# Kernel optimization log

Measured on AMD Instinct MI355X. Metric: run time of the kernel, lower is better.

## Reference

```python
import jax, jax.numpy as jnp
import numpy as np

B, NV, NH = 256, 512, 256


def setup_inputs() -> dict:
    key = jax.random.key(0)
    k1, k2, k3, k4, k5 = jax.random.split(key, 5)
    return {
        "wt": jax.random.normal(k1, (B, NH, NV), dtype=jnp.float32),
        "varh_diag": jax.random.uniform(k2, (B, NH), dtype=jnp.float32),
        "sig2": jax.random.uniform(k3, (B,), dtype=jnp.float32),
        "b": jax.random.normal(k4, (B, NV), dtype=jnp.float32),
        "muh": jax.random.normal(k5, (B, NH), dtype=jnp.float32),
    }


def reference(wt, varh_diag, sig2, b, muh):
    # wt: [B, nh, nv], varh_diag: [B, nh], sig2: [B], b: [B, nv], muh: [B, nh]
    nv = wt.shape[2]
    w = jnp.transpose(wt, (0, 2, 1))                      # [B, nv, nh]
    # diag(varh_diag) @ wt == broadcasted row scaling (avoids materializing diag)
    varvh = varh_diag[:, :, None] * wt                    # [B, nh, nv]
    # varv = w @ varh @ wt + sig2 * I
    varv = jnp.einsum('bvh,bhu->bvu', w, varvh)           # [B, nv, nv]
    varv = varv + sig2[:, None, None] * jnp.eye(nv, dtype=wt.dtype)
    # muv = b + w @ muh
    muv = b + jnp.einsum('bvh,bh->bv', w, muh)            # [B, nv]
    mu = jnp.concatenate([muv, muh], axis=1)              # [B, nv+nh]
    # block covariance: [[varv, varvh^T], [varvh, diag(varh_diag)]]
    varh = jax.vmap(jnp.diag)(varh_diag)                  # [B, nh, nh]
    varvht = jnp.transpose(varvh, (0, 2, 1))              # [B, nv, nh]
    top = jnp.concatenate([varv, varvht], axis=2)         # [B, nv, nv+nh]
    bot = jnp.concatenate([varvh, varh], axis=2)          # [B, nh, nv+nh]
    var = jnp.concatenate([top, bot], axis=1)             # [B, nv+nh, nv+nh]
    return mu, var
```

## Files before the change

kernel.cpp:

```cpp
#include <hip/hip_runtime.h>
#include <hip/hip_bf16.h>

#define B_  256
#define NH  256
#define NV  512
#define NT  768
#define TILES_PER_BATCH 22

typedef __bf16 bf16x8 __attribute__((ext_vector_type(8)));
typedef float  f32x4  __attribute__((ext_vector_type(4)));

__device__ __forceinline__ __bf16 f2bf(float f) { return static_cast<__bf16>(f); }

__global__ __launch_bounds__(256) void fused(const float* __restrict__ wt,
                                             const float* __restrict__ varh,
                                             const float* __restrict__ sig2,
                                             const float* __restrict__ bvec,
                                             const float* __restrict__ muh,
                                             float* __restrict__ out) {
    __shared__ __align__(16) char smem[38 * 1024];

    const int bid  = blockIdx.x;
    const int q    = bid >> 3;
    const int b    = (bid & 7) * 32 + q / TILES_PER_BATCH;
    const int tile = q % TILES_PER_BATCH;
    const int t    = threadIdx.x;

    const float* wtb  = wt + (size_t)b * NH * NV;
    float* mu   = out + (size_t)b * NT;
    float* varb = out + (size_t)B_ * NT + (size_t)b * NT * NT;

    if (tile < 10) {
        static const signed char MT[10] = {0,1,2,3, 0,0,0,1,1,2};
        static const signed char NTc[10] = {0,1,2,3, 1,2,3,2,3,3};
        const int mt = MT[tile], nt = NTc[tile];
        const bool diag = (mt == nt);

        bf16x8 (*As)[128]  = (bf16x8(*)[128])(smem);
        bf16x8 (*Bs)[128]  = (bf16x8(*)[128])(smem + 16 * 1024);
        float*  varh_s     = (float*)(smem + 32 * 1024);
        float*  muh_s      = (float*)(smem + 33 * 1024);
        float (*red)[128]  = (float(*)[128])(smem + 34 * 1024);

        const int m0 = mt * 128, n0 = nt * 128;
        const int lane = t & 63, wid = t >> 6;
        const int wm = wid >> 1, wn = wid & 1;
        const int mc = t & 31;
        const int kb = t >> 5;

        varh_s[t] = varh[b * NH + t];
        muh_s[t]  = muh[b * NH + t];

        f32x4 acc[4][4] = {};
        float acc_mu[4] = {0.f, 0.f, 0.f, 0.f};
        __syncthreads();

        for (int st = 0; st < 4; ++st) {
            const int k0 = st * 64;
            f32x4 av[8], bv[8];
            const float* baseA = wtb + (size_t)(k0 + kb * 8) * NV + m0 + 4 * mc;
#pragma unroll
            for (int j = 0; j < 8; ++j)
                av[j] = *reinterpret_cast<const f32x4*>(baseA + j * NV);
            if (!diag) {
                const float* baseB = wtb + (size_t)(k0 + kb * 8) * NV + n0 + 4 * mc;
#pragma unroll
                for (int j = 0; j < 8; ++j)
                    bv[j] = *reinterpret_cast<const f32x4*>(baseB + j * NV);
            } else {
#pragma unroll
                for (int j = 0; j < 8; ++j) bv[j] = av[j];
            }
            float sc[8];
#pragma unroll
            for (int j = 0; j < 8; ++j) sc[j] = varh_s[k0 + kb * 8 + j];

            if (diag) {
#pragma unroll
                for (int j = 0; j < 8; ++j) {
                    const float mh = muh_s[k0 + kb * 8 + j];
#pragma unroll
                    for (int mj = 0; mj < 4; ++mj) acc_mu[mj] += av[j][mj] * mh;
                }
            }

            if (st) __syncthreads();

#pragma unroll
            for (int mj = 0; mj < 4; ++mj) {
                bf16x8 pa, pb;
#pragma unroll
                for (int j = 0; j < 8; ++j) {
                    pa[j] = f2bf(av[j][mj]);
                    pb[j] = f2bf(bv[j][mj] * sc[j]);
                }
                const int ca = 4 * mc + mj;
                const int ci = ca ^ ((ca >> 3) & 7);
                As[kb][ci] = pa;
                Bs[kb][ci] = pb;
            }
            __syncthreads();

#pragma unroll
            for (int kh = 0; kh < 2; ++kh) {
                const int ko = kh * 4 + (lane >> 4);
                bf16x8 af[4], bfr[4];
#pragma unroll
                for (int f = 0; f < 4; ++f) {
                    const int mi = wm * 64 + f * 16 + (lane & 15);
                    af[f] = As[ko][mi ^ ((mi >> 3) & 7)];
                    const int ni = wn * 64 + f * 16 + (lane & 15);
                    bfr[f] = Bs[ko][ni ^ ((ni >> 3) & 7)];
                }
#pragma unroll
                for (int fm = 0; fm < 4; ++fm)
#pragma unroll
                    for (int fn = 0; fn < 4; ++fn)
                        acc[fm][fn] = __builtin_amdgcn_mfma_f32_16x16x32_bf16(
                            af[fm], bfr[fn], acc[fm][fn], 0, 0, 0);
            }
        }

        const float s2 = sig2[b];
#pragma unroll
        for (int fm = 0; fm < 4; ++fm) {
#pragma unroll
            for (int fn = 0; fn < 4; ++fn) {
                const int row = m0 + wm * 64 + fm * 16 + ((lane >> 4) << 2);
                const int col = n0 + wn * 64 + fn * 16 + (lane & 15);
#pragma unroll
                for (int r = 0; r < 4; ++r) {
                    float v = acc[fm][fn][r];
                    if (row + r == col) v += s2;
                    varb[(size_t)(row + r) * NT + col] = v;
                }
                if (!diag) {
                    *reinterpret_cast<f32x4*>(varb + (size_t)col * NT + row) =
                        acc[fm][fn];
                }
            }
        }

        if (diag) {
#pragma unroll
            for (int mj = 0; mj < 4; ++mj) red[kb][4 * mc + mj] = acc_mu[mj];
            __syncthreads();
            if (t < 128) {
                float s = 0.f;
#pragma unroll
                for (int k = 0; k < 8; ++k) s += red[k][t];
                mu[m0 + t] = bvec[b * NV + m0 + t] + s;
            }
        }
    } else if (tile < 18) {
        const int idx = tile - 10;
        const int hi = idx >> 2, vj = idx & 3;
        const int h0 = hi * 128, v0 = vj * 128;
        float (*tl)[65] = (float(*)[65])smem;
        const int r  = t >> 4;
        const int c4 = (t & 15) * 4;

        for (int sub = 0; sub < 4; ++sub) {
            const int sh = (sub >> 1) * 64, sv = (sub & 1) * 64;
            if (sub) __syncthreads();
#pragma unroll
            for (int p = 0; p < 4; ++p) {
                const int h = h0 + sh + r + 16 * p;
                const float vh = varh[b * NH + h];
                f32x4 x = *reinterpret_cast<const f32x4*>(
                    wtb + (size_t)h * NV + v0 + sv + c4);
                x *= vh;
                *reinterpret_cast<f32x4*>(
                    varb + (size_t)(NV + h) * NT + v0 + sv + c4) = x;
                tl[r + 16 * p][c4 + 0] = x[0];
                tl[r + 16 * p][c4 + 1] = x[1];
                tl[r + 16 * p][c4 + 2] = x[2];
                tl[r + 16 * p][c4 + 3] = x[3];
            }
            __syncthreads();
#pragma unroll
            for (int p = 0; p < 4; ++p) {
                const int vrow = v0 + sv + r + 16 * p;
                f32x4 y;
                y[0] = tl[c4 + 0][r + 16 * p];
                y[1] = tl[c4 + 1][r + 16 * p];
                y[2] = tl[c4 + 2][r + 16 * p];
                y[3] = tl[c4 + 3][r + 16 * p];
                *reinterpret_cast<f32x4*>(
                    varb + (size_t)vrow * NT + NV + h0 + sh + c4) = y;
            }
        }
    } else {
        const int d  = tile - 18;
        const int di = d >> 1, dj = d & 1;
        const int r0 = NV + di * 128, c0 = NV + dj * 128;
        const int rr = t >> 5;
        const int c4 = (t & 31) * 4;
#pragma unroll
        for (int p = 0; p < 16; ++p) {
            const int row = rr + 8 * p;
            f32x4 v = {0.f, 0.f, 0.f, 0.f};
            if (di == dj) {
                const int dpos = row - c4;
                if (dpos >= 0 && dpos < 4) v[dpos] = varh[b * NH + di * 128 + row];
            }
            *reinterpret_cast<f32x4*>(varb + (size_t)(r0 + row) * NT + c0 + c4) = v;
        }
        if (d == 0) mu[NV + t] = muh[b * NH + t];
    }
}

extern "C" void kernel_launch(void* const* d_in, const int* in_sizes, int n_in,
                              void* d_out, int out_size, void* d_ws, size_t ws_size,
                              hipStream_t stream) {
    (void)in_sizes; (void)n_in; (void)out_size; (void)d_ws; (void)ws_size;
    const float* wt   = (const float*)d_in[0];
    const float* varh = (const float*)d_in[1];
    const float* sig2 = (const float*)d_in[2];
    const float* bvec = (const float*)d_in[3];
    const float* muh  = (const float*)d_in[4];
    float* out = (float*)d_out;

    fused<<<B_ * TILES_PER_BATCH, 256, 0, stream>>>(wt, varh, sig2, bvec, muh, out);
}
```

Measured before the change: 162.4 us.

## Enlarge tiles to 256x256 with 512-thread blocks, 9 tiles per batch

The varv GEMM now uses three 256x256 upper-triangle tiles per batch instead of ten 128x128 tiles, run by 512-thread blocks with 8x4 MFMA accumulators per wave. The copy and diagonal tiles are resized to match, and the block count per batch drops from 22 to 9. This cuts redundant global reads of wt across tiles and the per-block overhead. In exchange, register pressure and LDS use (76KB) per block rise, which lowers occupancy, and the coarser tiles give fewer blocks to balance across CUs.

```diff
diff --git a/kernel.cpp b/kernel.cpp
--- a/kernel.cpp
+++ b/kernel.cpp
@@ -5,53 +5,51 @@
 #define NH  256
 #define NV  512
 #define NT  768
-#define TILES_PER_BATCH 22
+#define TPB 9
 
 typedef __bf16 bf16x8 __attribute__((ext_vector_type(8)));
 typedef float  f32x4  __attribute__((ext_vector_type(4)));
 
 __device__ __forceinline__ __bf16 f2bf(float f) { return static_cast<__bf16>(f); }
 
-__global__ __launch_bounds__(256) void fused(const float* __restrict__ wt,
+__global__ __launch_bounds__(512) void fused(const float* __restrict__ wt,
                                              const float* __restrict__ varh,
                                              const float* __restrict__ sig2,
                                              const float* __restrict__ bvec,
                                              const float* __restrict__ muh,
                                              float* __restrict__ out) {
-    __shared__ __align__(16) char smem[38 * 1024];
+    __shared__ __align__(16) char smem[76 * 1024];
 
     const int bid  = blockIdx.x;
     const int q    = bid >> 3;
-    const int b    = (bid & 7) * 32 + q / TILES_PER_BATCH;
-    const int tile = q % TILES_PER_BATCH;
+    const int b    = (bid & 7) * 32 + q / TPB;
+    const int tile = q % TPB;
     const int t    = threadIdx.x;
 
     const float* wtb  = wt + (size_t)b * NH * NV;
     float* mu   = out + (size_t)b * NT;
     float* varb = out + (size_t)B_ * NT + (size_t)b * NT * NT;
 
-    if (tile < 10) {
-        static const signed char MT[10] = {0,1,2,3, 0,0,0,1,1,2};
-        static const signed char NTc[10] = {0,1,2,3, 1,2,3,2,3,3};
-        const int mt = MT[tile], nt = NTc[tile];
-        const bool diag = (mt == nt);
-
-        bf16x8 (*As)[128]  = (bf16x8(*)[128])(smem);
-        bf16x8 (*Bs)[128]  = (bf16x8(*)[128])(smem + 16 * 1024);
-        float*  varh_s     = (float*)(smem + 32 * 1024);
-        float*  muh_s      = (float*)(smem + 33 * 1024);
-        float (*red)[128]  = (float(*)[128])(smem + 34 * 1024);
-
-        const int m0 = mt * 128, n0 = nt * 128;
+    if (tile < 3) {
+        const int  mt   = (tile == 1);
+        const int  nt   = (tile != 0);
+        const bool diag = (tile < 2);
+
+        bf16x8 (*As)[256] = (bf16x8(*)[256])(smem);
+        bf16x8 (*Bs)[256] = (bf16x8(*)[256])(smem + 32 * 1024);
+        float*  varh_s    = (float*)(smem + 64 * 1024);
+        float*  muh_s     = (float*)(smem + 65 * 1024);
+        float (*red)[256] = (float(*)[256])(smem + 66 * 1024);
+
+        const int m0 = mt * 256, n0 = nt * 256;
         const int lane = t & 63, wid = t >> 6;
-        const int wm = wid >> 1, wn = wid & 1;
-        const int mc = t & 31;
-        const int kb = t >> 5;
-
-        varh_s[t] = varh[b * NH + t];
-        muh_s[t]  = muh[b * NH + t];
-
-        f32x4 acc[4][4] = {};
+        const int wm = wid >> 2, wn = wid & 3;
+        const int mc = t & 63;
+        const int kb = t >> 6;
+
+        if (t < NH) { varh_s[t] = varh[b * NH + t]; muh_s[t] = muh[b * NH + t]; }
+
+        f32x4 acc[8][4] = {};
         float acc_mu[4] = {0.f, 0.f, 0.f, 0.f};
         __syncthreads();
 
@@ -67,9 +65,6 @@
 #pragma unroll
                 for (int j = 0; j < 8; ++j)
                     bv[j] = *reinterpret_cast<const f32x4*>(baseB + j * NV);
-            } else {
-#pragma unroll
-                for (int j = 0; j < 8; ++j) bv[j] = av[j];
             }
             float sc[8];
 #pragma unroll
@@ -91,8 +86,10 @@
                 bf16x8 pa, pb;
 #pragma unroll
                 for (int j = 0; j < 8; ++j) {
-                    pa[j] = f2bf(av[j][mj]);
-                    pb[j] = f2bf(bv[j][mj] * sc[j]);
+                    const float a  = av[j][mj];
+                    const float bb = diag ? a : bv[j][mj];
+                    pa[j] = f2bf(a);
+                    pb[j] = f2bf(bb * sc[j]);
                 }
                 const int ca = 4 * mc + mj;
                 const int ci = ca ^ ((ca >> 3) & 7);
@@ -104,29 +101,32 @@
 #pragma unroll
             for (int kh = 0; kh < 2; ++kh) {
                 const int ko = kh * 4 + (lane >> 4);
-                bf16x8 af[4], bfr[4];
+                bf16x8 af[8], bf4[4];
+#pragma unroll
+                for (int f = 0; f < 8; ++f) {
+                    const int mi = wm * 128 + f * 16 + (lane & 15);
+                    af[f] = As[ko][mi ^ ((mi >> 3) & 7)];
+                }
 #pragma unroll
                 for (int f = 0; f < 4; ++f) {
-                    const int mi = wm * 64 + f * 16 + (lane & 15);
-                    af[f] = As[ko][mi ^ ((mi >> 3) & 7)];
                     const int ni = wn * 64 + f * 16 + (lane & 15);
-                    bfr[f] = Bs[ko][ni ^ ((ni >> 3) & 7)];
-                }
-#pragma unroll
-                for (int fm = 0; fm < 4; ++fm)
+                    bf4[f] = Bs[ko][ni ^ ((ni >> 3) & 7)];
+                }
+#pragma unroll
+                for (int fm = 0; fm < 8; ++fm)
 #pragma unroll
                     for (int fn = 0; fn < 4; ++fn)
                         acc[fm][fn] = __builtin_amdgcn_mfma_f32_16x16x32_bf16(
-                            af[fm], bfr[fn], acc[fm][fn], 0, 0, 0);
+                            af[fm], bf4[fn], acc[fm][fn], 0, 0, 0);
             }
         }
 
         const float s2 = sig2[b];
 #pragma unroll
-        for (int fm = 0; fm < 4; ++fm) {
+        for (int fm = 0; fm < 8; ++fm) {
 #pragma unroll
             for (int fn = 0; fn < 4; ++fn) {
-                const int row = m0 + wm * 64 + fm * 16 + ((lane >> 4) << 2);
+                const int row = m0 + wm * 128 + fm * 16 + ((lane >> 4) << 2);
                 const int col = n0 + wn * 64 + fn * 16 + (lane & 15);
 #pragma unroll
                 for (int r = 0; r < 4; ++r) {
@@ -145,68 +145,70 @@
 #pragma unroll
             for (int mj = 0; mj < 4; ++mj) red[kb][4 * mc + mj] = acc_mu[mj];
             __syncthreads();
-            if (t < 128) {
+            if (t < 256) {
                 float s = 0.f;
 #pragma unroll
                 for (int k = 0; k < 8; ++k) s += red[k][t];
                 mu[m0 + t] = bvec[b * NV + m0 + t] + s;
             }
         }
-    } else if (tile < 18) {
-        const int idx = tile - 10;
-        const int hi = idx >> 2, vj = idx & 3;
-        const int h0 = hi * 128, v0 = vj * 128;
-        float (*tl)[65] = (float(*)[65])smem;
-        const int r  = t >> 4;
-        const int c4 = (t & 15) * 4;
-
-        for (int sub = 0; sub < 4; ++sub) {
-            const int sh = (sub >> 1) * 64, sv = (sub & 1) * 64;
-            if (sub) __syncthreads();
+    } else if (tile < 7) {
+        const int h0 = (tile - 3) * 64;
+        float (*tl)[64][65] = (float(*)[64][65])smem;
+        const int sub = t >> 8;
+        const int tt  = t & 255;
+        const int r   = tt >> 4;
+        const int c4  = (tt & 15) * 4;
+
+        for (int iter = 0; iter < 4; ++iter) {
+            const int v0 = iter * 128 + sub * 64;
+            if (iter) __syncthreads();
 #pragma unroll
             for (int p = 0; p < 4; ++p) {
-                const int h = h0 + sh + r + 16 * p;
+                const int h = h0 + r + 16 * p;
                 const float vh = varh[b * NH + h];
                 f32x4 x = *reinterpret_cast<const f32x4*>(
-                    wtb + (size_t)h * NV + v0 + sv + c4);
+                    wtb + (size_t)h * NV + v0 + c4);
                 x *= vh;
                 *reinterpret_cast<f32x4*>(
-                    varb + (size_t)(NV + h) * NT + v0 + sv + c4) = x;
-                tl[r + 16 * p][c4 + 0] = x[0];
-                tl[r + 16 * p][c4 + 1] = x[1];
-                tl[r + 16 * p][c4 + 2] = x[2];
-                tl[r + 16 * p][c4 + 3] = x[3];
+                    varb + (size_t)(NV + h) * NT + v0 + c4) = x;
+                tl[sub][r + 16 * p][c4 + 0] = x[0];
+                tl[sub][r + 16 * p][c4 + 1] = x[1];
+                tl[sub][r + 16 * p][c4 + 2] = x[2];
+                tl[sub][r + 16 * p][c4 + 3] = x[3];
             }
             __syncthreads();
 #pragma unroll
             for (int p = 0; p < 4; ++p) {
-                const int vrow = v0 + sv + r + 16 * p;
+                const int vrow = v0 + r + 16 * p;
                 f32x4 y;
-                y[0] = tl[c4 + 0][r + 16 * p];
-                y[1] = tl[c4 + 1][r + 16 * p];
-                y[2] = tl[c4 + 2][r + 16 * p];
-                y[3] = tl[c4 + 3][r + 16 * p];
+                y[0] = tl[sub][c4 + 0][r + 16 * p];
+                y[1] = tl[sub][c4 + 1][r + 16 * p];
+                y[2] = tl[sub][c4 + 2][r + 16 * p];
+                y[3] = tl[sub][c4 + 3][r + 16 * p];
                 *reinterpret_cast<f32x4*>(
-                    varb + (size_t)vrow * NT + NV + h0 + sh + c4) = y;
+                    varb + (size_t)vrow * NT + NV + h0 + c4) = y;
             }
         }
     } else {
-        const int d  = tile - 18;
-        const int di = d >> 1, dj = d & 1;
-        const int r0 = NV + di * 128, c0 = NV + dj * 128;
-        const int rr = t >> 5;
-        const int c4 = (t & 31) * 4;
+        const int d  = tile - 7;
+        const int r0 = NV + d * 128;
+        const int rr = t >> 6;
+        const int c4 = (t & 63) * 4;
 #pragma unroll
         for (int p = 0; p < 16; ++p) {
             const int row = rr + 8 * p;
-            f32x4 v = {0.f, 0.f, 0.f, 0.f};
-            if (di == dj) {
-                const int dpos = row - c4;
-                if (dpos >= 0 && dpos < 4) v[dpos] = varh[b * NH + di * 128 + row];
-            }
-            *reinterpret_cast<f32x4*>(varb + (size_t)(r0 + row) * NT + c0 + c4) = v;
-        }
-        if (d == 0) mu[NV + t] = muh[b * NH + t];
+            const int g   = d * 128 + row;
+            const int dpos = g - c4;
+            const float val = (dpos >= 0 && dpos < 4) ? varh[b * NH + g] : 0.f;
+            f32x4 v;
+            v[0] = (dpos == 0) ? val : 0.f;
+            v[1] = (dpos == 1) ? val : 0.f;
+            v[2] = (dpos == 2) ? val : 0.f;
+            v[3] = (dpos == 3) ? val : 0.f;
+            *reinterpret_cast<f32x4*>(varb + (size_t)(r0 + row) * NT + NV + c4) = v;
+        }
+        if (d == 0 && t < NH) mu[NV + t] = muh[b * NH + t];
     }
 }
 
@@ -221,5 +223,5 @@
     const float* muh  = (const float*)d_in[4];
     float* out = (float*)d_out;
 
-    fused<<<B_ * TILES_PER_BATCH, 256, 0, stream>>>(wt, varh, sig2, bvec, muh, out);
+    fused<<<B_ * TPB, 512, 0, stream>>>(wt, varh, sig2, bvec, muh, out);
 }
```

Result: no change. 161.9 us (-0.4%).
